# Optimization experiments

Measured on AMD Instinct MI355X. Metric: run time of the kernel, lower is better.

## Reference

```python
import jax, jax.numpy as jnp
import numpy as np

B, S, I, H = 128, 1024, 512, 1024


def setup_inputs() -> dict:
    key = jax.random.key(0)
    k0, k1, k2, k3, k4, k5 = jax.random.split(key, 6)
    bound = 1.0 / np.sqrt(H)  # PyTorch LSTMCell init range
    sequence = jax.random.normal(k0, (B, S, I), dtype=jnp.float32)
    input_length = jax.random.randint(k1, (B,), 1, S + 1)  # at least length 1
    W_ih = jax.random.uniform(k2, (4 * H, I), minval=-bound, maxval=bound, dtype=jnp.float32)
    W_hh = jax.random.uniform(k3, (4 * H, H), minval=-bound, maxval=bound, dtype=jnp.float32)
    b_ih = jax.random.uniform(k4, (4 * H,), minval=-bound, maxval=bound, dtype=jnp.float32)
    b_hh = jax.random.uniform(k5, (4 * H,), minval=-bound, maxval=bound, dtype=jnp.float32)
    return {"sequence": sequence, "input_length": input_length,
            "W_ih": W_ih, "W_hh": W_hh, "b_ih": b_ih, "b_hh": b_hh}


def reference(sequence, input_length, W_ih, W_hh, b_ih, b_hh):
    # LSTM acceptor: run LSTMCell over time, return hidden state at t = len-1.
    batch, seq_len, _ = sequence.shape
    hidden = W_hh.shape[1]
    h0 = jnp.zeros((batch, hidden), sequence.dtype)
    c0 = jnp.zeros((batch, hidden), sequence.dtype)
    last0 = jnp.zeros((batch, hidden), sequence.dtype)
    last_step = input_length - 1  # [B]

    def step(carry, xs):
        h, c, last = carry
        x_t, t = xs  # x_t: [B, I]
        gates = x_t @ W_ih.T + b_ih + h @ W_hh.T + b_hh  # [B, 4H]
        i_g, f_g, g_g, o_g = jnp.split(gates, 4, axis=-1)  # PyTorch order i,f,g,o
        c = jax.nn.sigmoid(f_g) * c + jax.nn.sigmoid(i_g) * jnp.tanh(g_g)
        h = jax.nn.sigmoid(o_g) * jnp.tanh(c)
        last = jnp.where((t == last_step)[:, None], h, last)
        return (h, c, last), None

    xs = (jnp.swapaxes(sequence, 0, 1), jnp.arange(seq_len, dtype=input_length.dtype))
    (h, c, last), _ = jax.lax.scan(step, (h0, c0, last0), xs)
    return last
```

## Files before the change

### kernel.cpp

```cpp
#include <hip/hip_runtime.h>
#include <hip/hip_bf16.h>
#include <math.h>

#define B_   128
#define S_   1024
#define I_   512
#define H_   1024
#define NWG  256
#define NTHR 512
#define LDA  1544

typedef __bf16 v8bf __attribute__((ext_vector_type(8)));
typedef float  v4f  __attribute__((ext_vector_type(4)));

__device__ __forceinline__ v8bf cvt8(const float4 a, const float4 b) {
    v8bf r;
    r[0] = (__bf16)a.x; r[1] = (__bf16)a.y; r[2] = (__bf16)a.z; r[3] = (__bf16)a.w;
    r[4] = (__bf16)b.x; r[5] = (__bf16)b.y; r[6] = (__bf16)b.z; r[7] = (__bf16)b.w;
    return r;
}

__device__ __forceinline__ float sigm(float x) { return 1.f / (1.f + __expf(-x)); }
__device__ __forceinline__ float tanh_fast(float x) {
    const float xc = fminf(fmaxf(x, -15.f), 15.f);
    const float e  = __expf(2.f * xc);
    return (e - 1.f) / (e + 1.f);
}

__global__ __launch_bounds__(NTHR, 1) void lstm_persist(
    const float* __restrict__ seq, const int* __restrict__ len,
    const float* __restrict__ Wih, const float* __restrict__ Whh,
    const float* __restrict__ bih, const float* __restrict__ bhh,
    float* __restrict__ out, __bf16* __restrict__ hA, __bf16* __restrict__ hB,
    unsigned* __restrict__ cnt)
{
    __shared__ __bf16 Apan[16 * LDA];
    __shared__ float  glds[4][2][16][33];

    const int wg   = blockIdx.x;
    const int bg   = wg >> 5;
    const int cg   = wg & 31;
    const int tid  = threadIdx.x;
    const int lane = tid & 63;
    const int wv   = tid >> 6;
    const int l15  = lane & 15;
    const int q    = lane >> 4;
    const int gate = wv >> 1;
    const int ks   = wv & 1;

    const int n0   = gate * H_ + cg * 32;
    const int col0 = n0 + l15;
    const int col1 = n0 + 16 + l15;

    v8bf w0[24], w1[24];
    #pragma unroll
    for (int j = 0; j < 24; ++j) {
        const int kt = ks * 24 + j;
        const int k  = kt * 32 + q * 8;
        if (kt < 16) {
            const float4* p0 = (const float4*)&Wih[(size_t)col0 * I_ + k];
            const float4* p1 = (const float4*)&Wih[(size_t)col1 * I_ + k];
            w0[j] = cvt8(p0[0], p0[1]);
            w1[j] = cvt8(p1[0], p1[1]);
        } else {
            const float4* p0 = (const float4*)&Whh[(size_t)col0 * H_ + (k - I_)];
            const float4* p1 = (const float4*)&Whh[(size_t)col1 * H_ + (k - I_)];
            w0[j] = cvt8(p0[0], p0[1]);
            w1[j] = cvt8(p1[0], p1[1]);
        }
    }
    const float b0 = ks ? 0.f : (bih[col0] + bhh[col0]);
    const float b1 = ks ? 0.f : (bih[col1] + bhh[col1]);

    const int cb = tid >> 5;
    const int cc = tid & 31;
    const int gb = bg * 16 + cb;
    const int gc = cg * 32 + cc;
    const int mylen = len[gb];
    float creg = 0.f;

    unsigned* mycnt = cnt + (size_t)bg * S_;

    for (int t = 0; t < S_; ++t) {
        const __bf16* hrd = (t & 1) ? hA : hB;
        __bf16*       hwr = (t & 1) ? hB : hA;

        {
            const float4* xp = (const float4*)&seq[((size_t)gb * S_ + (size_t)t) * I_ + cc * 16];
            v8bf* dx = (v8bf*)&Apan[cb * LDA + cc * 16];
            const float4 x0 = xp[0], x1 = xp[1];
            dx[0] = cvt8(x0, x1);
            const float4 x2 = xp[2], x3 = xp[3];
            dx[1] = cvt8(x2, x3);
        }

        if (t > 0 && tid == 0) {
            while (__hip_atomic_load(&mycnt[t - 1], __ATOMIC_RELAXED,
                                     __HIP_MEMORY_SCOPE_AGENT) < 32u) {
                __builtin_amdgcn_s_sleep(1);
            }
        }
        __syncthreads();
        asm volatile("" ::: "memory");

        {
            const unsigned long long* hs =
                (const unsigned long long*)(hrd + (size_t)(bg * 16) * H_);
            unsigned long long vals[8];
            #pragma unroll
            for (int j = 0; j < 8; ++j)
                vals[j] = __hip_atomic_load(&hs[cb * 256 + cc + 32 * j],
                                            __ATOMIC_RELAXED, __HIP_MEMORY_SCOPE_AGENT);
            #pragma unroll
            for (int j = 0; j < 8; ++j)
                *(unsigned long long*)&Apan[cb * LDA + I_ + 4 * (cc + 32 * j)] = vals[j];
        }
        __syncthreads();

        v4f acc0 = {0.f, 0.f, 0.f, 0.f};
        v4f acc1 = {0.f, 0.f, 0.f, 0.f};
        const __bf16* ap = &Apan[l15 * LDA + ks * 768 + q * 8];
        #pragma unroll
        for (int j = 0; j < 24; ++j) {
            const v8bf a = *(const v8bf*)(ap + j * 32);
            acc0 = __builtin_amdgcn_mfma_f32_16x16x32_bf16(a, w0[j], acc0, 0, 0, 0);
            acc1 = __builtin_amdgcn_mfma_f32_16x16x32_bf16(a, w1[j], acc1, 0, 0, 0);
        }

        #pragma unroll
        for (int r = 0; r < 4; ++r) {
            glds[gate][ks][q * 4 + r][l15]      = acc0[r] + b0;
            glds[gate][ks][q * 4 + r][16 + l15] = acc1[r] + b1;
        }
        __syncthreads();

        const float ig = glds[0][0][cb][cc] + glds[0][1][cb][cc];
        const float fg = glds[1][0][cb][cc] + glds[1][1][cb][cc];
        const float gg = glds[2][0][cb][cc] + glds[2][1][cb][cc];
        const float og = glds[3][0][cb][cc] + glds[3][1][cb][cc];

        const float cn = sigm(fg) * creg + sigm(ig) * tanh_fast(gg);
        const float hv = sigm(og) * tanh_fast(cn);
        creg = cn;

        const __bf16 hb = (__bf16)hv;
        const unsigned short us = __builtin_bit_cast(unsigned short, hb);
        const unsigned nb = __shfl_xor((unsigned)us, 1);
        if ((lane & 1) == 0) {
            const unsigned pair = (unsigned)us | (nb << 16);
            __hip_atomic_store((unsigned*)&hwr[(size_t)gb * H_ + gc], pair,
                               __ATOMIC_RELAXED, __HIP_MEMORY_SCOPE_AGENT);
        }
        if (t == mylen - 1) out[(size_t)gb * H_ + gc] = hv;

        __syncthreads();
        if (tid == 0) {
            __hip_atomic_fetch_add(&mycnt[t], 1u, __ATOMIC_RELAXED,
                                   __HIP_MEMORY_SCOPE_AGENT);
        }
    }
}

extern "C" void kernel_launch(void* const* d_in, const int* in_sizes, int n_in,
                              void* d_out, int out_size, void* d_ws, size_t ws_size,
                              hipStream_t stream) {
    const float* seq = (const float*)d_in[0];
    const int*   len = (const int*)d_in[1];
    const float* Wih = (const float*)d_in[2];
    const float* Whh = (const float*)d_in[3];
    const float* bih = (const float*)d_in[4];
    const float* bhh = (const float*)d_in[5];
    float* out = (float*)d_out;

    char* ws = (char*)d_ws;
    unsigned* cnt = (unsigned*)ws;
    __bf16* hA   = (__bf16*)(ws + 32768);
    __bf16* hB   = (__bf16*)(ws + 32768 + 262144);

    hipMemsetAsync(cnt, 0, 8 * S_ * sizeof(unsigned), stream);
    hipMemsetAsync(hA, 0, (size_t)B_ * H_ * 2 * sizeof(__bf16), stream);

    void* args[] = {(void*)&seq, (void*)&len, (void*)&Wih, (void*)&Whh,
                    (void*)&bih, (void*)&bhh, (void*)&out, (void*)&hA,
                    (void*)&hB, (void*)&cnt};
    hipError_t e = hipLaunchCooperativeKernel((void*)lstm_persist, dim3(NWG),
                                              dim3(NTHR), args, 0, stream);
    if (e != hipSuccess) {
        lstm_persist<<<dim3(NWG), dim3(NTHR), 0, stream>>>(seq, len, Wih, Whh,
                                                           bih, bhh, out, hA, hB, cnt);
    }
}
```

Baseline: 3.598 ms.

## Overlap input-projection MFMAs with h wait, spread counters, prepack bf16 weights

Adds a pre-pass kernel that converts W_ih and W_hh into one concatenated bf16 matrix, so the persistent kernel loads its register-resident weights directly. The per-step GEMM is split into the x-part and the h-part: the x-projection MFMAs run while the h loads from the previous step are still in flight, and the h tile is written to LDS only afterwards. The single per-batch-group step counter becomes four counters keyed by column-group parity that the waiter sums, which reduces atomic contention. The workgroup-to-(batch, column) mapping is also transposed and the launch bounds raised to 2, at the cost of an extra launch and more polling loads per spin.

```diff
diff --git a/kernel.cpp b/kernel.cpp
--- a/kernel.cpp
+++ b/kernel.cpp
@@ -6,6 +6,7 @@
 #define S_   1024
 #define I_   512
 #define H_   1024
+#define KC   1536
 #define NWG  256
 #define NTHR 512
 #define LDA  1544
@@ -27,9 +28,21 @@
     return (e - 1.f) / (e + 1.f);
 }
 
-__global__ __launch_bounds__(NTHR, 1) void lstm_persist(
+__global__ void lstm_pack(const float* __restrict__ Wih, const float* __restrict__ Whh,
+                          __bf16* __restrict__ Wc)
+{
+    const size_t e = ((size_t)blockIdx.x * 256 + threadIdx.x) * 8;
+    const int col = (int)(e / KC);
+    const int k   = (int)(e % KC);
+    const float4* src = (k < I_) ? (const float4*)&Wih[(size_t)col * I_ + k]
+                                 : (const float4*)&Whh[(size_t)col * H_ + (k - I_)];
+    const float4 a = src[0], b = src[1];
+    *(v8bf*)&Wc[e] = cvt8(a, b);
+}
+
+__global__ __launch_bounds__(NTHR, 2) void lstm_persist(
     const float* __restrict__ seq, const int* __restrict__ len,
-    const float* __restrict__ Wih, const float* __restrict__ Whh,
+    const __bf16* __restrict__ Wc,
     const float* __restrict__ bih, const float* __restrict__ bhh,
     float* __restrict__ out, __bf16* __restrict__ hA, __bf16* __restrict__ hB,
     unsigned* __restrict__ cnt)
@@ -38,8 +51,8 @@
     __shared__ float  glds[4][2][16][33];
 
     const int wg   = blockIdx.x;
-    const int bg   = wg >> 5;
-    const int cg   = wg & 31;
+    const int bg   = wg & 7;
+    const int cg   = wg >> 3;
     const int tid  = threadIdx.x;
     const int lane = tid & 63;
     const int wv   = tid >> 6;
@@ -52,22 +65,28 @@
     const int col0 = n0 + l15;
     const int col1 = n0 + 16 + l15;
 
-    v8bf w0[24], w1[24];
-    #pragma unroll
-    for (int j = 0; j < 24; ++j) {
-        const int kt = ks * 24 + j;
-        const int k  = kt * 32 + q * 8;
-        if (kt < 16) {
-            const float4* p0 = (const float4*)&Wih[(size_t)col0 * I_ + k];
-            const float4* p1 = (const float4*)&Wih[(size_t)col1 * I_ + k];
-            w0[j] = cvt8(p0[0], p0[1]);
-            w1[j] = cvt8(p1[0], p1[1]);
-        } else {
-            const float4* p0 = (const float4*)&Whh[(size_t)col0 * H_ + (k - I_)];
-            const float4* p1 = (const float4*)&Whh[(size_t)col1 * H_ + (k - I_)];
-            w0[j] = cvt8(p0[0], p0[1]);
-            w1[j] = cvt8(p1[0], p1[1]);
-        }
+    v8bf wx0[8], wx1[8], wh0[16], wh1[16];
+    {
+        const __bf16* wr0 = Wc + (size_t)col0 * KC;
+        const __bf16* wr1 = Wc + (size_t)col1 * KC;
+        const int xo = ks * 256 + q * 8;
+        const int ho = I_ + ks * 512 + q * 8;
+        #pragma unroll
+        for (int j = 0; j < 8; ++j) {
+            wx0[j] = *(const v8bf*)(wr0 + xo + j * 32);
+            wx1[j] = *(const v8bf*)(wr1 + xo + j * 32);
+        }
+        #pragma unroll
+        for (int j = 0; j < 16; ++j) {
+            wh0[j] = *(const v8bf*)(wr0 + ho + j * 32);
+            wh1[j] = *(const v8bf*)(wr1 + ho + j * 32);
+        }
+        #pragma unroll
+        for (int j = 0; j < 8; ++j)
+            asm volatile("" : "+v"(wx0[j]), "+v"(wx1[j]));
+        #pragma unroll
+        for (int j = 0; j < 16; ++j)
+            asm volatile("" : "+v"(wh0[j]), "+v"(wh1[j]));
     }
     const float b0 = ks ? 0.f : (bih[col0] + bhh[col0]);
     const float b1 = ks ? 0.f : (bih[col1] + bhh[col1]);
@@ -79,8 +98,6 @@
     const int mylen = len[gb];
     float creg = 0.f;
 
-    unsigned* mycnt = cnt + (size_t)bg * S_;
-
     for (int t = 0; t < S_; ++t) {
         const __bf16* hrd = (t & 1) ? hA : hB;
         __bf16*       hwr = (t & 1) ? hB : hA;
@@ -95,36 +112,52 @@
         }
 
         if (t > 0 && tid == 0) {
-            while (__hip_atomic_load(&mycnt[t - 1], __ATOMIC_RELAXED,
-                                     __HIP_MEMORY_SCOPE_AGENT) < 32u) {
-                __builtin_amdgcn_s_sleep(1);
-            }
-        }
-        __syncthreads();
-        asm volatile("" ::: "memory");
-
+            const unsigned* c0 = cnt + ((size_t)(t - 1) * 4) * 32 + bg;
+            unsigned s;
+            do {
+                s  = __hip_atomic_load(c0 +  0, __ATOMIC_RELAXED, __HIP_MEMORY_SCOPE_AGENT);
+                s += __hip_atomic_load(c0 + 32, __ATOMIC_RELAXED, __HIP_MEMORY_SCOPE_AGENT);
+                s += __hip_atomic_load(c0 + 64, __ATOMIC_RELAXED, __HIP_MEMORY_SCOPE_AGENT);
+                s += __hip_atomic_load(c0 + 96, __ATOMIC_RELAXED, __HIP_MEMORY_SCOPE_AGENT);
+            } while (s < 32u);
+        }
+        __syncthreads();
+
+        unsigned long long hv8[8];
         {
             const unsigned long long* hs =
                 (const unsigned long long*)(hrd + (size_t)(bg * 16) * H_);
-            unsigned long long vals[8];
             #pragma unroll
             for (int j = 0; j < 8; ++j)
-                vals[j] = __hip_atomic_load(&hs[cb * 256 + cc + 32 * j],
-                                            __ATOMIC_RELAXED, __HIP_MEMORY_SCOPE_AGENT);
-            #pragma unroll
-            for (int j = 0; j < 8; ++j)
-                *(unsigned long long*)&Apan[cb * LDA + I_ + 4 * (cc + 32 * j)] = vals[j];
-        }
-        __syncthreads();
+                hv8[j] = __hip_atomic_load(&hs[cb * 256 + cc + 32 * j],
+                                           __ATOMIC_RELAXED, __HIP_MEMORY_SCOPE_AGENT);
+        }
 
         v4f acc0 = {0.f, 0.f, 0.f, 0.f};
         v4f acc1 = {0.f, 0.f, 0.f, 0.f};
-        const __bf16* ap = &Apan[l15 * LDA + ks * 768 + q * 8];
-        #pragma unroll
-        for (int j = 0; j < 24; ++j) {
-            const v8bf a = *(const v8bf*)(ap + j * 32);
-            acc0 = __builtin_amdgcn_mfma_f32_16x16x32_bf16(a, w0[j], acc0, 0, 0, 0);
-            acc1 = __builtin_amdgcn_mfma_f32_16x16x32_bf16(a, w1[j], acc1, 0, 0, 0);
+        {
+            const __bf16* ap = &Apan[l15 * LDA + ks * 256 + q * 8];
+            #pragma unroll
+            for (int j = 0; j < 8; ++j) {
+                const v8bf a = *(const v8bf*)(ap + j * 32);
+                acc0 = __builtin_amdgcn_mfma_f32_16x16x32_bf16(a, wx0[j], acc0, 0, 0, 0);
+                acc1 = __builtin_amdgcn_mfma_f32_16x16x32_bf16(a, wx1[j], acc1, 0, 0, 0);
+            }
+        }
+
+        #pragma unroll
+        for (int j = 0; j < 8; ++j)
+            *(unsigned long long*)&Apan[cb * LDA + I_ + 4 * (cc + 32 * j)] = hv8[j];
+        __syncthreads();
+
+        {
+            const __bf16* ap = &Apan[l15 * LDA + I_ + ks * 512 + q * 8];
+            #pragma unroll
+            for (int j = 0; j < 16; ++j) {
+                const v8bf a = *(const v8bf*)(ap + j * 32);
+                acc0 = __builtin_amdgcn_mfma_f32_16x16x32_bf16(a, wh0[j], acc0, 0, 0, 0);
+                acc1 = __builtin_amdgcn_mfma_f32_16x16x32_bf16(a, wh1[j], acc1, 0, 0, 0);
+            }
         }
 
         #pragma unroll
@@ -154,10 +187,9 @@
         if (t == mylen - 1) out[(size_t)gb * H_ + gc] = hv;
 
         __syncthreads();
-        if (tid == 0) {
-            __hip_atomic_fetch_add(&mycnt[t], 1u, __ATOMIC_RELAXED,
-                                   __HIP_MEMORY_SCOPE_AGENT);
-        }
+        if (tid == 0)
+            __hip_atomic_fetch_add(cnt + ((size_t)t * 4 + (cg & 3)) * 32 + bg, 1u,
+                                   __ATOMIC_RELAXED, __HIP_MEMORY_SCOPE_AGENT);
     }
 }
 
@@ -173,20 +205,22 @@
     float* out = (float*)d_out;
 
     char* ws = (char*)d_ws;
-    unsigned* cnt = (unsigned*)ws;
-    __bf16* hA   = (__bf16*)(ws + 32768);
-    __bf16* hB   = (__bf16*)(ws + 32768 + 262144);
-
-    hipMemsetAsync(cnt, 0, 8 * S_ * sizeof(unsigned), stream);
-    hipMemsetAsync(hA, 0, (size_t)B_ * H_ * 2 * sizeof(__bf16), stream);
-
-    void* args[] = {(void*)&seq, (void*)&len, (void*)&Wih, (void*)&Whh,
-                    (void*)&bih, (void*)&bhh, (void*)&out, (void*)&hA,
-                    (void*)&hB, (void*)&cnt};
+    __bf16*   Wc  = (__bf16*)ws;
+    __bf16*   hA  = (__bf16*)(ws + 12582912);
+    __bf16*   hB  = (__bf16*)(ws + 12845056);
+    unsigned* cnt = (unsigned*)(ws + 13107200);
+
+    hipMemsetAsync(hA, 0, 2 * (size_t)B_ * H_ * sizeof(__bf16), stream);
+    hipMemsetAsync(cnt, 0, (size_t)S_ * 4 * 32 * sizeof(unsigned), stream);
+
+    lstm_pack<<<dim3(3072), dim3(256), 0, stream>>>(Wih, Whh, Wc);
+
+    void* args[] = {(void*)&seq, (void*)&len, (void*)&Wc, (void*)&bih,
+                    (void*)&bhh, (void*)&out, (void*)&hA, (void*)&hB, (void*)&cnt};
     hipError_t e = hipLaunchCooperativeKernel((void*)lstm_persist, dim3(NWG),
                                               dim3(NTHR), args, 0, stream);
     if (e != hipSuccess) {
-        lstm_persist<<<dim3(NWG), dim3(NTHR), 0, stream>>>(seq, len, Wih, Whh,
-                                                           bih, bhh, out, hA, hB, cnt);
+        lstm_persist<<<dim3(NWG), dim3(NTHR), 0, stream>>>(seq, len, Wc, bih,
+                                                           bhh, out, hA, hB, cnt);
     }
 }
```

New measurement: 3.352 ms. 1.07x faster.
